# Kernel optimization log

Hardware: AMD Instinct MI355X
Metric: run time of the kernel (lower is better)

## Reference

```python
import jax, jax.numpy as jnp
import numpy as np

N_NODES = 100000

def setup_inputs() -> dict:
    key = jax.random.key(0)
    k1, k2, k3 = jax.random.split(key, 3)
    R, C, E = 8, 4, 2000000
    weight = jax.random.normal(k1, (R, C), dtype=jnp.float32) * 0.01
    edge_index = jax.random.randint(k2, (R, 2, E), 0, N_NODES, dtype=jnp.int64)
    edge_value = jax.random.uniform(k3, (R, E), dtype=jnp.float32)
    return {"weight": weight, "edge_index": edge_index, "edge_value": edge_value}

def reference(weight, edge_index, edge_value):
    # weight: [R, C]; edge_index: [R, 2, E]; edge_value: [R, E]
    R, C = weight.shape
    E = edge_value.shape[1]
    # softmax over relations (dim 0), matching F.softmax(self.weight, dim=0)
    filt = jax.nn.softmax(weight, axis=0)  # [R, C]
    # For each out-channel i: concat over relations j of edge_value[j] * filt[j, i]
    # -> values [C, R*E]; edge index concat is identical for every channel.
    vals = (filt.T[:, :, None] * edge_value[None, :, :]).reshape(C, R * E)
    total_edge_index = jnp.transpose(edge_index, (1, 0, 2)).reshape(2, R * E)
    return total_edge_index, vals
```

## Files before the change

kernel.cpp:

```cpp
#include <hip/hip_runtime.h>


#define GT_E  2000000
#define GT_R  8
#define GT_C  4
#define GT_RE (GT_R * GT_E)

__global__ __launch_bounds__(256) void gt_idx_kernel(const int* __restrict__ idx,
                                                     float* __restrict__ out) {
    long long t = (long long)blockIdx.x * 256 + threadIdx.x;
    long long v = t * 4;
    if (v >= 2LL * GT_RE) return;
    int s   = (int)(v / GT_RE);
    int rem = (int)(v - (long long)s * GT_RE);
    int j   = rem / GT_E;
    int e   = rem - j * GT_E;
    long long in_off = (long long)j * (2 * GT_E) + (long long)s * GT_E + e;
    const int4 iv = *(const int4*)(idx + in_off);
    float4 f;
    f.x = (float)iv.x; f.y = (float)iv.y; f.z = (float)iv.z; f.w = (float)iv.w;
    *(float4*)(out + v) = f;
}

__global__ __launch_bounds__(256) void gt_vals_kernel(const float* __restrict__ w,
                                                      const float* __restrict__ ev,
                                                      float* __restrict__ out) {
    __shared__ float filt[GT_R * GT_C];
    if (threadIdx.x < GT_C) {
        int i = threadIdx.x;
        float col[GT_R];
        float m = -1e30f;
        #pragma unroll
        for (int j = 0; j < GT_R; ++j) { col[j] = w[j * GT_C + i]; m = fmaxf(m, col[j]); }
        float sum = 0.f;
        #pragma unroll
        for (int j = 0; j < GT_R; ++j) { col[j] = expf(col[j] - m); sum += col[j]; }
        float inv = 1.f / sum;
        #pragma unroll
        for (int j = 0; j < GT_R; ++j) filt[j * GT_C + i] = col[j] * inv;
    }
    __syncthreads();

    long long t = (long long)blockIdx.x * 256 + threadIdx.x;
    long long v = t * 4;
    if (v >= (long long)GT_C * GT_RE) return;
    int i   = (int)(v / GT_RE);
    int rem = (int)(v - (long long)i * GT_RE);
    int j   = rem / GT_E;
    int e   = rem - j * GT_E;
    const float4 x = *(const float4*)(ev + (long long)j * GT_E + e);
    float f = filt[j * GT_C + i];
    float4 r;
    r.x = x.x * f; r.y = x.y * f; r.z = x.z * f; r.w = x.w * f;
    *(float4*)(out + 2LL * GT_RE + v) = r;
}

extern "C" void kernel_launch(void* const* d_in, const int* in_sizes, int n_in,
                              void* d_out, int out_size, void* d_ws, size_t ws_size,
                              hipStream_t stream) {
    const float* weight     = (const float*)d_in[0];
    const int*   edge_index = (const int*)d_in[1];
    const float* edge_value = (const float*)d_in[2];
    float* out = (float*)d_out;

    gt_idx_kernel<<<31250, 256, 0, stream>>>(edge_index, out);
    gt_vals_kernel<<<62500, 256, 0, stream>>>(weight, edge_value, out);
}
```

Before: 520.8 us.

## Fuse index conversion and value scaling into one grid-stride kernel

```diff
diff --git a/kernel.cpp b/kernel.cpp
--- a/kernel.cpp
+++ b/kernel.cpp
@@ -5,26 +5,16 @@
 #define GT_R  8
 #define GT_C  4
 #define GT_RE (GT_R * GT_E)
+#define GT_E4 (GT_E / 4)
+#define GT_CHUNKS (GT_R * GT_E4)
 
-__global__ __launch_bounds__(256) void gt_idx_kernel(const int* __restrict__ idx,
-                                                     float* __restrict__ out) {
-    long long t = (long long)blockIdx.x * 256 + threadIdx.x;
-    long long v = t * 4;
-    if (v >= 2LL * GT_RE) return;
-    int s   = (int)(v / GT_RE);
-    int rem = (int)(v - (long long)s * GT_RE);
-    int j   = rem / GT_E;
-    int e   = rem - j * GT_E;
-    long long in_off = (long long)j * (2 * GT_E) + (long long)s * GT_E + e;
-    const int4 iv = *(const int4*)(idx + in_off);
-    float4 f;
-    f.x = (float)iv.x; f.y = (float)iv.y; f.z = (float)iv.z; f.w = (float)iv.w;
-    *(float4*)(out + v) = f;
-}
+typedef float f32x4 __attribute__((ext_vector_type(4)));
+typedef int   i32x4 __attribute__((ext_vector_type(4)));
 
-__global__ __launch_bounds__(256) void gt_vals_kernel(const float* __restrict__ w,
-                                                      const float* __restrict__ ev,
-                                                      float* __restrict__ out) {
+__global__ __launch_bounds__(256) void gt_fused_kernel(const float* __restrict__ w,
+                                                       const int*   __restrict__ idx,
+                                                       const float* __restrict__ ev,
+                                                       float*       __restrict__ out) {
     __shared__ float filt[GT_R * GT_C];
     if (threadIdx.x < GT_C) {
         int i = threadIdx.x;
@@ -41,18 +31,31 @@
     }
     __syncthreads();
 
-    long long t = (long long)blockIdx.x * 256 + threadIdx.x;
-    long long v = t * 4;
-    if (v >= (long long)GT_C * GT_RE) return;
-    int i   = (int)(v / GT_RE);
-    int rem = (int)(v - (long long)i * GT_RE);
-    int j   = rem / GT_E;
-    int e   = rem - j * GT_E;
-    const float4 x = *(const float4*)(ev + (long long)j * GT_E + e);
-    float f = filt[j * GT_C + i];
-    float4 r;
-    r.x = x.x * f; r.y = x.y * f; r.z = x.z * f; r.w = x.w * f;
-    *(float4*)(out + 2LL * GT_RE + v) = r;
+    const int stride = (int)gridDim.x * 256;
+    for (int c = (int)blockIdx.x * 256 + (int)threadIdx.x; c < GT_CHUNKS; c += stride) {
+        const int j  = c / GT_E4;
+        const int e  = (c - j * GT_E4) * 4;
+        const int in_base = j * (2 * GT_E) + e;
+        const int je      = j * GT_E + e;
+
+        const i32x4 i0 = __builtin_nontemporal_load((const i32x4*)(idx + in_base));
+        const i32x4 i1 = __builtin_nontemporal_load((const i32x4*)(idx + in_base + GT_E));
+        const f32x4 v  = __builtin_nontemporal_load((const f32x4*)(ev + je));
+
+        const f32x4 a = __builtin_convertvector(i0, f32x4);
+        const f32x4 b = __builtin_convertvector(i1, f32x4);
+        __builtin_nontemporal_store(a, (f32x4*)(out + je));
+        __builtin_nontemporal_store(b, (f32x4*)(out + GT_RE + je));
+
+        const float f0 = filt[j * GT_C + 0];
+        const float f1 = filt[j * GT_C + 1];
+        const float f2 = filt[j * GT_C + 2];
+        const float f3 = filt[j * GT_C + 3];
+        __builtin_nontemporal_store(v * f0, (f32x4*)(out + 2 * GT_RE + je));
+        __builtin_nontemporal_store(v * f1, (f32x4*)(out + 3 * GT_RE + je));
+        __builtin_nontemporal_store(v * f2, (f32x4*)(out + 4 * GT_RE + je));
+        __builtin_nontemporal_store(v * f3, (f32x4*)(out + 5 * GT_RE + je));
+    }
 }
 
 extern "C" void kernel_launch(void* const* d_in, const int* in_sizes, int n_in,
@@ -63,6 +66,5 @@
     const float* edge_value = (const float*)d_in[2];
     float* out = (float*)d_out;
 
-    gt_idx_kernel<<<31250, 256, 0, stream>>>(edge_index, out);
-    gt_vals_kernel<<<62500, 256, 0, stream>>>(weight, edge_value, out);
+    gt_fused_kernel<<<2048, 256, 0, stream>>>(weight, edge_index, edge_value, out);
 }
```

Result: faster. 500.9 us (-3.8%).
